# Performance work log

Hardware: AMD Instinct MI355X
Metric: run time of the kernel (lower is better)

## Reference

```python
import jax, jax.numpy as jnp
from jax import lax
import numpy as np

B, N = 512, 256
INF = jnp.float32(1e30)


def setup_inputs() -> dict:
    key = jax.random.key(0)
    k1, k2 = jax.random.split(key)
    costs = jax.random.normal(k1, (B, N, N), dtype=jnp.float32)
    pad_mask = jax.random.randint(k2, (B, N), 0, 2).astype(bool)
    return {"costs": costs, "pad_mask": pad_mask}


def _solve_lap(cost):
    """Jonker-Volgenant shortest-augmenting-path LAP, same math as
    scipy.optimize.linear_sum_assignment. cost: [n, n], rows=objects,
    cols=predictions. Returns col4row[n]: assigned column per row."""
    n = cost.shape[0]
    idx = jnp.arange(n, dtype=jnp.int32)

    def assign_row(cur_row, state):
        u, v, col4row, row4col = state
        cur_row = jnp.int32(cur_row)

        def path_cond(c):
            return c[2] < 0

        def path_body(c):
            i, minval, sink, shortest, pathrow, SR, SC = c
            SR = SR.at[i].set(True)
            r = minval + cost[i] - u[i] - v  # reduced cost of extending path via row i
            upd = jnp.logical_and(~SC, r < shortest)
            shortest = jnp.where(upd, r, shortest)
            pathrow = jnp.where(upd, i, pathrow)
            masked = jnp.where(SC, INF, shortest)
            j = jnp.argmin(masked).astype(jnp.int32)
            minval = masked[j]
            SC = SC.at[j].set(True)
            nxt = row4col[j]
            sink = jnp.where(nxt < 0, j, jnp.int32(-1))
            i = jnp.where(nxt < 0, i, nxt)
            return (i, minval, sink, shortest, pathrow, SR, SC)

        init = (cur_row, jnp.float32(0.0), jnp.int32(-1),
                jnp.full((n,), INF, jnp.float32),
                jnp.full((n,), -1, jnp.int32),
                jnp.zeros((n,), bool), jnp.zeros((n,), bool))
        i, minval, sink, shortest, pathrow, SR, SC = lax.while_loop(
            path_cond, path_body, init)

        # dual updates (Crouse 2016 / scipy lsap)
        u = u.at[cur_row].add(minval)
        others = jnp.logical_and(SR, idx != cur_row)
        u = u + jnp.where(others, minval - shortest[jnp.clip(col4row, 0, n - 1)], 0.0)
        v = v - jnp.where(SC, minval - shortest, 0.0)

        # augment along the alternating path back to cur_row
        def aug_cond(c):
            return ~c[3]

        def aug_body(c):
            j, col4row, row4col, done = c
            i = pathrow[j]
            row4col = row4col.at[j].set(i)
            j_next = col4row[i]
            col4row = col4row.at[i].set(j)
            return (j_next, col4row, row4col, i == cur_row)

        _, col4row, row4col, _ = lax.while_loop(
            aug_cond, aug_body, (sink, col4row, row4col, jnp.bool_(False)))
        return (u, v, col4row, row4col)

    state = (jnp.zeros((n,), jnp.float32), jnp.zeros((n,), jnp.float32),
             jnp.full((n,), -1, jnp.int32), jnp.full((n,), -1, jnp.int32))
    _, _, col4row, _ = lax.fori_loop(0, n, assign_row, state)
    return col4row


def _match_one(cost_t, n_k):
    # cost_t: [n_obj_slots, n_pred] (== costs[k].T); n_k: number of valid objects
    n = cost_t.shape[0]
    idx = jnp.arange(n, dtype=jnp.int32)
    rows_valid = idx < n_k
    # padded object rows get constant cost -> assignment of real rows unchanged
    P = jnp.where(rows_valid[:, None], cost_t, 0.0)
    cols = _solve_lap(P)
    # prediction indices used by real objects (cols is a permutation)
    used = jnp.zeros((n,), bool).at[cols].set(rows_valid)
    # unused prediction indices, ascending, placed first
    order = jnp.argsort(jnp.where(used, idx + n, idx)).astype(jnp.int32)
    fill = order[jnp.clip(idx - n_k, 0, n - 1)]
    return jnp.where(rows_valid, cols, fill)


def _forward(costs, pad_mask):
    costs = jnp.nan_to_num(costs.astype(jnp.float32),
                           nan=1e6, posinf=1e6, neginf=1e6)
    n_k = jnp.sum(pad_mask, axis=1).astype(jnp.int32)  # valid objects per batch
    cost_t = jnp.swapaxes(costs, 1, 2)                 # [B, n_obj, n_pred]
    return jax.vmap(_match_one)(cost_t, n_k)


def reference(costs, pad_mask):
    return _forward(costs, pad_mask)
```

## Files before the change

### kernel.cpp

```cpp
#include <hip/hip_runtime.h>
#include <math.h>

#define NB 512
#define NN 256
#define NCACHE 60
#define LAP_INF 1e30f

#define WS_NK_OFF 1024
#define WS_RMV_OFF 8192
#define WS_RMA_OFF (8192 + 512 * 1024)
#define WS_PT_OFF_FULL (8192 + 1024 * 1024)
#define WS_PT_OFF_R4 8192

__global__ __launch_bounds__(1024)
void detect_kernel(const unsigned int* __restrict__ pw, int* __restrict__ flag) {
  __shared__ int notInt, notFloat;
  if (threadIdx.x == 0) { notInt = 0; notFloat = 0; }
  __syncthreads();
  int li = 0, lf = 0;
  for (int t = threadIdx.x; t < 32768; t += 1024) {
    unsigned int w = pw[t];
    if (w > 1u) li = 1;
    if (w != 0u && w != 0x3F800000u) lf = 1;
  }
  if (li) atomicOr(&notInt, 1);
  if (lf) atomicOr(&notFloat, 1);
  __syncthreads();
  if (threadIdx.x == 0) flag[0] = (!notInt) ? 1 : ((!notFloat) ? 2 : 0);
}

__global__ __launch_bounds__(64)
void nk_kernel(const void* __restrict__ pm, const int* __restrict__ flag,
               int* __restrict__ nk) {
  const int k = blockIdx.x;
  const int lane = threadIdx.x;
  const int fl = flag[0];
  int cnt4 = 0;
  if (fl == 1) {
    const int* p = ((const int*)pm) + k * NN;
#pragma unroll
    for (int q = 0; q < 4; ++q) cnt4 += (p[lane * 4 + q] != 0);
  } else if (fl == 2) {
    const float* p = ((const float*)pm) + k * NN;
#pragma unroll
    for (int q = 0; q < 4; ++q) cnt4 += (p[lane * 4 + q] != 0.0f);
  } else {
    const unsigned char* p = ((const unsigned char*)pm) + k * NN;
#pragma unroll
    for (int q = 0; q < 4; ++q) cnt4 += (p[lane * 4 + q] != 0);
  }
#pragma unroll
  for (int off = 32; off > 0; off >>= 1) cnt4 += __shfl_down(cnt4, off);
  if (lane == 0) nk[k] = cnt4;
}

__global__ __launch_bounds__(256)
void transpose_kernel(const float* __restrict__ in, float* __restrict__ out,
                      const int* __restrict__ nk) {
  const int k = blockIdx.z;
  const int i0 = blockIdx.x * 32;
  int bnd = nk[k];
  bnd = bnd > NCACHE ? bnd : NCACHE;
  if (i0 >= bnd) return;
  __shared__ float tile[32][33];
  const float* A = in + ((size_t)k << 16);
  float* Bp = out + ((size_t)k << 16);
  const int tx = threadIdx.x, ty = threadIdx.y;
  const int j0 = blockIdx.y * 32;
#pragma unroll
  for (int r = 0; r < 32; r += 8) {
    float x = A[(size_t)(j0 + ty + r) * NN + (i0 + tx)];
    tile[ty + r][tx] = isfinite(x) ? x : 1e6f;
  }
  __syncthreads();
#pragma unroll
  for (int r = 0; r < 32; r += 8) {
    Bp[(size_t)(i0 + ty + r) * NN + (j0 + tx)] = tile[tx][ty + r];
  }
}

template <int CTRL>
__device__ __forceinline__ unsigned dpp_min_step(unsigned x) {
  unsigned y = (unsigned)__builtin_amdgcn_update_dpp((int)x, (int)x, CTRL, 0xF, 0xF, false);
  return y < x ? y : x;
}
__device__ __forceinline__ unsigned wave_min_u32(unsigned x) {
  x = dpp_min_step<0xB1>(x);
  x = dpp_min_step<0x4E>(x);
  x = dpp_min_step<0x141>(x);
  x = dpp_min_step<0x140>(x);
  x = dpp_min_step<0x142>(x);
  x = dpp_min_step<0x143>(x);
  return (unsigned)__builtin_amdgcn_readlane((int)x, 63);
}
__device__ __forceinline__ unsigned f2o(float f) {
  unsigned x = __float_as_uint(f);
  return x ^ ((unsigned)((int)x >> 31) | 0x80000000u);
}
__device__ __forceinline__ float o2f(unsigned m) {
  unsigned x = (m & 0x80000000u) ? (m & 0x7FFFFFFFu) : ~m;
  return __uint_as_float(x);
}
__device__ __forceinline__ int sel4(const int a[4], int s) {
  return (s == 0) ? a[0] : (s == 1) ? a[1] : (s == 2) ? a[2] : a[3];
}
__device__ __forceinline__ void set4(int a[4], int s, int v) {
  if (s == 0) a[0] = v; else if (s == 1) a[1] = v;
  else if (s == 2) a[2] = v; else a[3] = v;
}
__device__ __forceinline__ void setf4(float a[4], int s, float v) {
  if (s == 0) a[0] = v; else if (s == 1) a[1] = v;
  else if (s == 2) a[2] = v; else a[3] = v;
}

__global__ __launch_bounds__(256)
void rowmin_kernel(const float* __restrict__ Pt, const int* __restrict__ nk,
                   float* __restrict__ rmv, int* __restrict__ rma) {
  const int k = blockIdx.x;
  const int wid = threadIdx.x >> 6, lane = threadIdx.x & 63;
  const int row = blockIdx.y * 4 + wid;
  int bnd = nk[k];
  bnd = bnd > NCACHE ? bnd : NCACHE;
  if (row >= bnd) return;
  const float4 rv = *(const float4*)(Pt + ((size_t)k << 16) + (size_t)row * NN + lane * 4);
  float bv = rv.x; int bj = lane * 4;
  if (rv.y < bv) { bv = rv.y; bj = lane * 4 + 1; }
  if (rv.z < bv) { bv = rv.z; bj = lane * 4 + 2; }
  if (rv.w < bv) { bv = rv.w; bj = lane * 4 + 3; }
  const unsigned m = f2o(bv);
  const unsigned g = wave_min_u32(m);
  const unsigned long long cm = __ballot(m == g);
  const int owner = __ffsll(cm) - 1;
  const int ja = __builtin_amdgcn_readlane(bj, owner);
  if (lane == 0) {
    rmv[k * NN + row] = o2f(g);
    rma[k * NN + row] = ja;
  }
}

__global__ __launch_bounds__(64)
void lap_kernel(const float* __restrict__ costs, const void* __restrict__ pm,
                const int* __restrict__ flag, const int* __restrict__ nkArr,
                const float* __restrict__ rmv, const int* __restrict__ rma,
                const float* __restrict__ Pt, int* __restrict__ out, int mode) {
  const int k = blockIdx.x;
  const int lane = threadIdx.x;

  __shared__ __align__(16) float rowCache[NCACHE][NN];
  __shared__ float shortestL[NN];
  __shared__ int freeRowsL[NN];
  __shared__ unsigned char used[NN];

  const float* PtK = Pt + ((size_t)k << 16);
  const float* costK = costs + ((size_t)k << 16);

  int n_k;
  if (mode >= 1) {
    n_k = nkArr[k];
  } else {
    const int fl = flag[0];
    int cnt4 = 0;
    if (fl == 1) {
      const int* p = ((const int*)pm) + k * NN;
#pragma unroll
      for (int q = 0; q < 4; ++q) cnt4 += (p[lane * 4 + q] != 0);
    } else if (fl == 2) {
      const float* p = ((const float*)pm) + k * NN;
#pragma unroll
      for (int q = 0; q < 4; ++q) cnt4 += (p[lane * 4 + q] != 0.0f);
    } else {
      const unsigned char* p = ((const unsigned char*)pm) + k * NN;
#pragma unroll
      for (int q = 0; q < 4; ++q) cnt4 += (p[lane * 4 + q] != 0);
    }
#pragma unroll
    for (int off = 32; off > 0; off >>= 1) cnt4 += __shfl_down(cnt4, off);
    n_k = __shfl(cnt4, 0);
  }

  if (mode >= 1) {
    const float4* s4 = (const float4*)PtK;
    float4* c4 = (float4*)rowCache;
    for (int t = lane; t < NCACHE * (NN / 4); t += 64) c4[t] = s4[t];
  } else {
    for (int e = lane; e < NCACHE * NN; e += 64) {
      const int i = e >> 8, j = e & 255;
      float x = costK[(size_t)j * NN + i];
      rowCache[i][j] = isfinite(x) ? x : 1e6f;
    }
  }

  float vv[4] = {0.f, 0.f, 0.f, 0.f};
  float uu[4] = {0.f, 0.f, 0.f, 0.f};
  int r4c[4] = {-1, -1, -1, -1};
  int c4r[4] = {-1, -1, -1, -1};
  int ja[4] = {-1, -1, -1, -1};
  int nfree = 0;
  __syncthreads();

  if (mode == 2) {
    const float4 mv = *(const float4*)(rmv + k * NN + lane * 4);
    const int4 av = *(const int4*)(rma + k * NN + lane * 4);
    uu[0] = mv.x; uu[1] = mv.y; uu[2] = mv.z; uu[3] = mv.w;
    ja[0] = av.x; ja[1] = av.y; ja[2] = av.z; ja[3] = av.w;
#pragma unroll
    for (int q = 0; q < 4; ++q)
      if (lane * 4 + q >= n_k) uu[q] = 0.f;
    for (int r = 0; r < n_k; ++r) {
      const int js = __builtin_amdgcn_readlane(sel4(ja, r & 3), r >> 2);
      const int occ = __builtin_amdgcn_readlane(sel4(r4c, js & 3), js >> 2);
      if (occ < 0) {
        if (lane == (js >> 2)) set4(r4c, js & 3, r);
        if (lane == (r >> 2)) set4(c4r, r & 3, js);
      } else {
        if (lane == 0) freeRowsL[nfree] = r;
        nfree++;
      }
    }
  } else {
    float4 carry = {0.f, 0.f, 0.f, 0.f};
    for (int r = 0; r < n_k; ++r) {
      float cc[4];
      if (r < NCACHE) {
        const float4 rv = *(const float4*)(&rowCache[r][lane * 4]);
        cc[0] = rv.x; cc[1] = rv.y; cc[2] = rv.z; cc[3] = rv.w;
      } else if (mode >= 1) {
        cc[0] = carry.x; cc[1] = carry.y; cc[2] = carry.z; cc[3] = carry.w;
      } else {
#pragma unroll
        for (int q = 0; q < 4; ++q) {
          float x = costK[(size_t)(lane * 4 + q) * NN + r];
          cc[q] = isfinite(x) ? x : 1e6f;
        }
      }
      if (mode >= 1 && r + 1 >= NCACHE && r + 1 < n_k)
        carry = *(const float4*)(PtK + (size_t)(r + 1) * NN + lane * 4);

      unsigned lbv = 0xFFFFFFFFu;
      int lbq = 0;
#pragma unroll
      for (int q = 0; q < 4; ++q) {
        const unsigned m = f2o(cc[q]);
        if (m < lbv) { lbv = m; lbq = q; }
      }
      const unsigned gv = wave_min_u32(lbv);
      const unsigned long long cmask = __ballot(lbv == gv);
      const int owner = __ffsll((unsigned long long)cmask) - 1;
      const int js = (owner << 2) + __builtin_amdgcn_readlane(lbq, owner);
      if (lane == (r >> 2)) setf4(uu, r & 3, o2f(gv));
      const int occ = __builtin_amdgcn_readlane(sel4(r4c, js & 3), owner);
      if (occ < 0) {
        if (lane == owner) set4(r4c, js & 3, r);
        if (lane == (r >> 2)) set4(c4r, r & 3, js);
      } else {
        if (lane == 0) freeRowsL[nfree] = r;
        nfree++;
      }
    }
  }
  __syncthreads();

  for (int t = 0; t < nfree; ++t) {
    const int cur = freeRowsL[t];
    float sh[4] = {LAP_INF, LAP_INF, LAP_INF, LAP_INF};
    int pr[4] = {-1, -1, -1, -1};
    unsigned scm = 0;
    unsigned srm = 0;
    float minval = 0.f;
    int i = cur, sink = -1;

    while (sink < 0) {
      const int islot = i & 3, iowner = i >> 2;
      if (lane == iowner) srm |= (1u << islot);
      const float su = (islot == 0) ? uu[0] : (islot == 1) ? uu[1]
                     : (islot == 2) ? uu[2] : uu[3];
      const float ui = __int_as_float(
          __builtin_amdgcn_readlane(__float_as_int(su), iowner));

      float cc[4];
      if (i < NCACHE) {
        const float4 rv = *(const float4*)(&rowCache[i][lane * 4]);
        cc[0] = rv.x; cc[1] = rv.y; cc[2] = rv.z; cc[3] = rv.w;
      } else if (mode >= 1) {
        const float4 rv = *(const float4*)(PtK + (size_t)i * NN + lane * 4);
        cc[0] = rv.x; cc[1] = rv.y; cc[2] = rv.z; cc[3] = rv.w;
      } else {
#pragma unroll
        for (int q = 0; q < 4; ++q) {
          float x = costK[(size_t)(lane * 4 + q) * NN + i];
          cc[q] = isfinite(x) ? x : 1e6f;
        }
      }

      unsigned lbv = 0xFFFFFFFFu;
      int lbq = 0;
#pragma unroll
      for (int q = 0; q < 4; ++q) {
        float r = minval + cc[q];
        r = r - ui;
        r = r - vv[q];
        const bool sc = (scm >> q) & 1u;
        if (!sc && r < sh[q]) { sh[q] = r; pr[q] = i; }
        const unsigned m = sc ? 0xFFFFFFFFu : f2o(sh[q]);
        if (m < lbv) { lbv = m; lbq = q; }
      }
      const unsigned gv = wave_min_u32(lbv);
      minval = o2f(gv);
      const unsigned long long cmask = __ballot(lbv == gv);
      const int owner = __ffsll((unsigned long long)cmask) - 1;
      const int js = (owner << 2) + __builtin_amdgcn_readlane(lbq, owner);
      if (lane == owner) scm |= (1u << lbq);
      const int nxt = __builtin_amdgcn_readlane(sel4(r4c, js & 3), owner);
      if (nxt < 0) sink = js; else i = nxt;
    }

#pragma unroll
    for (int q = 0; q < 4; ++q) shortestL[lane * 4 + q] = sh[q];
    __syncthreads();

#pragma unroll
    for (int q = 0; q < 4; ++q) {
      if ((srm >> q) & 1u) {
        const int row = lane * 4 + q;
        if (row == cur) uu[q] = uu[q] + minval;
        else uu[q] = uu[q] + (minval - shortestL[c4r[q]]);
      }
      if ((scm >> q) & 1u) vv[q] = vv[q] - (minval - sh[q]);
    }

    int j = sink;
    bool done = false;
    while (!done) {
      const int pi = __builtin_amdgcn_readlane(sel4(pr, j & 3), j >> 2);
      if (lane == (j >> 2)) set4(r4c, j & 3, pi);
      const int jn = __builtin_amdgcn_readlane(sel4(c4r, pi & 3), pi >> 2);
      if (lane == (pi >> 2)) set4(c4r, pi & 3, j);
      done = (pi == cur);
      j = jn;
    }
    __syncthreads();
  }

  for (int t = lane; t < NN; t += 64) used[t] = 0;
  __syncthreads();
#pragma unroll
  for (int q = 0; q < 4; ++q) {
    const int row = lane * 4 + q;
    if (row < n_k) used[c4r[q]] = 1;
  }
  __syncthreads();
  int* outK = out + k * NN;
#pragma unroll
  for (int q = 0; q < 4; ++q) {
    const int row = lane * 4 + q;
    if (row < n_k) outK[row] = c4r[q];
  }
  if (lane == 0) {
    int pos = n_k;
    for (int c = 0; c < NN; ++c)
      if (!used[c]) outK[pos++] = c;
  }
}

extern "C" void kernel_launch(void* const* d_in, const int* in_sizes, int n_in,
                              void* d_out, int out_size, void* d_ws, size_t ws_size,
                              hipStream_t stream) {
  const float* costs = (const float*)d_in[0];
  const void* pm = d_in[1];
  int* out = (int*)d_out;

  int* flag = (int*)d_ws;
  int* nk = (int*)((char*)d_ws + WS_NK_OFF);
  const size_t ptBytes = (size_t)NB * NN * NN * sizeof(float);

  int mode;
  float* rmv; int* rma; float* Pt;
  if (ws_size >= WS_PT_OFF_FULL + ptBytes) {
    mode = 2;
    rmv = (float*)((char*)d_ws + WS_RMV_OFF);
    rma = (int*)((char*)d_ws + WS_RMA_OFF);
    Pt = (float*)((char*)d_ws + WS_PT_OFF_FULL);
  } else if (ws_size >= WS_PT_OFF_R4 + ptBytes) {
    mode = 1;
    rmv = (float*)d_ws; rma = (int*)d_ws;
    Pt = (float*)((char*)d_ws + WS_PT_OFF_R4);
  } else {
    mode = 0;
    rmv = (float*)d_ws; rma = (int*)d_ws;
    Pt = (float*)costs;
  }

  detect_kernel<<<1, 1024, 0, stream>>>((const unsigned int*)pm, flag);
  nk_kernel<<<NB, 64, 0, stream>>>(pm, flag, nk);
  if (mode >= 1) {
    dim3 g(8, 8, NB), b(32, 8);
    transpose_kernel<<<g, b, 0, stream>>>(costs, Pt, nk);
  }
  if (mode == 2) {
    dim3 g(NB, 64);
    rowmin_kernel<<<g, 256, 0, stream>>>(Pt, nk, rmv, rma);
  }
  lap_kernel<<<NB, 64, 0, stream>>>(costs, pm, flag, nk, rmv, rma, Pt, out, mode);
}
```

Baseline: 406.6 us.

## Add auction-style augmenting row reduction before shortest-path phase

Adds a Jonker-Volgenant augmenting row reduction pass: each free row takes its two smallest reduced costs, lowers a column price and steals the column, requeueing any displaced row, capped at a fixed number of steps. Row top-two minima are precomputed by the rowmin kernel and used as a fast path while the relevant columns are unmodified. The goal is to leave fewer free rows for the expensive shortest-augmenting-path loop. It also removes the separate nk kernel by computing counts inline in each kernel, and raises the shared row cache from 60 to 64 rows. The extra reduction pass and the more complex price bookkeeping could cost more than they save.

```diff
diff --git a/kernel.cpp b/kernel.cpp
--- a/kernel.cpp
+++ b/kernel.cpp
@@ -3,14 +3,16 @@
 
 #define NB 512
 #define NN 256
-#define NCACHE 60
+#define NCACHE 64
 #define LAP_INF 1e30f
-
-#define WS_NK_OFF 1024
-#define WS_RMV_OFF 8192
-#define WS_RMA_OFF (8192 + 512 * 1024)
-#define WS_PT_OFF_FULL (8192 + 1024 * 1024)
-#define WS_PT_OFF_R4 8192
+#define ARR_CAP 512
+
+#define WS_RM1_OFF 8192
+#define WS_RJ1_OFF (8192 + (1 << 19))
+#define WS_RM2_OFF (8192 + (2 << 19))
+#define WS_RJ2_OFF (8192 + 3 * (1 << 19))
+#define WS_PT_OFF (8192 + (4 << 19))
+#define WS_PT_OFF_MIN 8192
 
 __global__ __launch_bounds__(1024)
 void detect_kernel(const unsigned int* __restrict__ pw, int* __restrict__ flag) {
@@ -27,56 +29,6 @@
   if (lf) atomicOr(&notFloat, 1);
   __syncthreads();
   if (threadIdx.x == 0) flag[0] = (!notInt) ? 1 : ((!notFloat) ? 2 : 0);
-}
-
-__global__ __launch_bounds__(64)
-void nk_kernel(const void* __restrict__ pm, const int* __restrict__ flag,
-               int* __restrict__ nk) {
-  const int k = blockIdx.x;
-  const int lane = threadIdx.x;
-  const int fl = flag[0];
-  int cnt4 = 0;
-  if (fl == 1) {
-    const int* p = ((const int*)pm) + k * NN;
-#pragma unroll
-    for (int q = 0; q < 4; ++q) cnt4 += (p[lane * 4 + q] != 0);
-  } else if (fl == 2) {
-    const float* p = ((const float*)pm) + k * NN;
-#pragma unroll
-    for (int q = 0; q < 4; ++q) cnt4 += (p[lane * 4 + q] != 0.0f);
-  } else {
-    const unsigned char* p = ((const unsigned char*)pm) + k * NN;
-#pragma unroll
-    for (int q = 0; q < 4; ++q) cnt4 += (p[lane * 4 + q] != 0);
-  }
-#pragma unroll
-  for (int off = 32; off > 0; off >>= 1) cnt4 += __shfl_down(cnt4, off);
-  if (lane == 0) nk[k] = cnt4;
-}
-
-__global__ __launch_bounds__(256)
-void transpose_kernel(const float* __restrict__ in, float* __restrict__ out,
-                      const int* __restrict__ nk) {
-  const int k = blockIdx.z;
-  const int i0 = blockIdx.x * 32;
-  int bnd = nk[k];
-  bnd = bnd > NCACHE ? bnd : NCACHE;
-  if (i0 >= bnd) return;
-  __shared__ float tile[32][33];
-  const float* A = in + ((size_t)k << 16);
-  float* Bp = out + ((size_t)k << 16);
-  const int tx = threadIdx.x, ty = threadIdx.y;
-  const int j0 = blockIdx.y * 32;
-#pragma unroll
-  for (int r = 0; r < 32; r += 8) {
-    float x = A[(size_t)(j0 + ty + r) * NN + (i0 + tx)];
-    tile[ty + r][tx] = isfinite(x) ? x : 1e6f;
-  }
-  __syncthreads();
-#pragma unroll
-  for (int r = 0; r < 32; r += 8) {
-    Bp[(size_t)(i0 + ty + r) * NN + (j0 + tx)] = tile[tx][ty + r];
-  }
 }
 
 template <int CTRL>
@@ -112,71 +64,150 @@
   if (s == 0) a[0] = v; else if (s == 1) a[1] = v;
   else if (s == 2) a[2] = v; else a[3] = v;
 }
+__device__ __forceinline__ void subf4(float a[4], int s, float d) {
+  if (s == 0) a[0] -= d; else if (s == 1) a[1] -= d;
+  else if (s == 2) a[2] -= d; else a[3] -= d;
+}
+
+__device__ __forceinline__ void wave_two_smallest(
+    int lane, unsigned lm1, int lj1, unsigned lm2, int lj2,
+    unsigned& g1, int& gj1, unsigned& g2, int& gj2) {
+  g1 = wave_min_u32(lm1);
+  const unsigned long long b1 = __ballot(lm1 == g1);
+  const int o1 = __ffsll(b1) - 1;
+  gj1 = __builtin_amdgcn_readlane(lj1, o1);
+  const unsigned c = (lane == o1) ? lm2 : lm1;
+  const int cj = (lane == o1) ? lj2 : lj1;
+  g2 = wave_min_u32(c);
+  const unsigned long long b2 = __ballot(c == g2);
+  const int o2 = __ffsll(b2) - 1;
+  gj2 = __builtin_amdgcn_readlane(cj, o2);
+}
+
+__device__ __forceinline__ int wave_nk(const void* pm, int fl, int k, int lane) {
+  int cnt4 = 0;
+  if (fl == 1) {
+    const int* p = ((const int*)pm) + k * NN;
+#pragma unroll
+    for (int q = 0; q < 4; ++q) cnt4 += (p[lane * 4 + q] != 0);
+  } else if (fl == 2) {
+    const float* p = ((const float*)pm) + k * NN;
+#pragma unroll
+    for (int q = 0; q < 4; ++q) cnt4 += (p[lane * 4 + q] != 0.0f);
+  } else {
+    const unsigned char* p = ((const unsigned char*)pm) + k * NN;
+#pragma unroll
+    for (int q = 0; q < 4; ++q) cnt4 += (p[lane * 4 + q] != 0);
+  }
+#pragma unroll
+  for (int off = 32; off > 0; off >>= 1) cnt4 += __shfl_down(cnt4, off);
+  return __shfl(cnt4, 0);
+}
 
 __global__ __launch_bounds__(256)
-void rowmin_kernel(const float* __restrict__ Pt, const int* __restrict__ nk,
-                   float* __restrict__ rmv, int* __restrict__ rma) {
+void transpose_kernel(const float* __restrict__ in, float* __restrict__ out,
+                      const void* __restrict__ pm, const int* __restrict__ flag) {
+  __shared__ float tile[32][33];
+  __shared__ int bndS;
+  const int k = blockIdx.z;
+  const int fl = flag[0];
+  int bit;
+  if (fl == 1) bit = (((const int*)pm)[k * NN + threadIdx.x] != 0);
+  else if (fl == 2) bit = (((const float*)pm)[k * NN + threadIdx.x] != 0.0f);
+  else bit = (((const unsigned char*)pm)[k * NN + threadIdx.x] != 0);
+  const unsigned long long bb = __ballot(bit);
+  if (threadIdx.x == 0) bndS = 0;
+  __syncthreads();
+  if ((threadIdx.x & 63) == 0) atomicAdd(&bndS, __popcll(bb));
+  __syncthreads();
+  int bnd = bndS;
+  bnd = bnd > NCACHE ? bnd : NCACHE;
+  const int i0 = blockIdx.x * 32;
+  if (i0 >= bnd) return;
+  const float* A = in + ((size_t)k << 16);
+  float* Bp = out + ((size_t)k << 16);
+  const int tx = threadIdx.x & 31, ty = threadIdx.x >> 5;
+  const int j0 = blockIdx.y * 32;
+#pragma unroll
+  for (int r = 0; r < 32; r += 8) {
+    float x = A[(size_t)(j0 + ty + r) * NN + (i0 + tx)];
+    tile[ty + r][tx] = isfinite(x) ? x : 1e6f;
+  }
+  __syncthreads();
+#pragma unroll
+  for (int r = 0; r < 32; r += 8) {
+    Bp[(size_t)(i0 + ty + r) * NN + (j0 + tx)] = tile[tx][ty + r];
+  }
+}
+
+__global__ __launch_bounds__(256)
+void rowmin_kernel(const float* __restrict__ Pt, const void* __restrict__ pm,
+                   const int* __restrict__ flag,
+                   float* __restrict__ rm1, int* __restrict__ rj1,
+                   float* __restrict__ rm2, int* __restrict__ rj2) {
   const int k = blockIdx.x;
   const int wid = threadIdx.x >> 6, lane = threadIdx.x & 63;
   const int row = blockIdx.y * 4 + wid;
-  int bnd = nk[k];
-  bnd = bnd > NCACHE ? bnd : NCACHE;
+  const int fl = flag[0];
+  const int n_k = wave_nk(pm, fl, k, lane);
+  int bnd = n_k > NCACHE ? n_k : NCACHE;
   if (row >= bnd) return;
   const float4 rv = *(const float4*)(Pt + ((size_t)k << 16) + (size_t)row * NN + lane * 4);
-  float bv = rv.x; int bj = lane * 4;
-  if (rv.y < bv) { bv = rv.y; bj = lane * 4 + 1; }
-  if (rv.z < bv) { bv = rv.z; bj = lane * 4 + 2; }
-  if (rv.w < bv) { bv = rv.w; bj = lane * 4 + 3; }
-  const unsigned m = f2o(bv);
-  const unsigned g = wave_min_u32(m);
-  const unsigned long long cm = __ballot(m == g);
-  const int owner = __ffsll(cm) - 1;
-  const int ja = __builtin_amdgcn_readlane(bj, owner);
+  float w[4] = {rv.x, rv.y, rv.z, rv.w};
+  unsigned lm1 = 0xFFFFFFFFu, lm2 = 0xFFFFFFFFu;
+  int lj1 = 0, lj2 = 0;
+#pragma unroll
+  for (int q = 0; q < 4; ++q) {
+    const unsigned m = f2o(w[q]);
+    const int c = lane * 4 + q;
+    if (m < lm1) { lm2 = lm1; lj2 = lj1; lm1 = m; lj1 = c; }
+    else if (m < lm2) { lm2 = m; lj2 = c; }
+  }
+  unsigned g1, g2; int gj1, gj2;
+  wave_two_smallest(lane, lm1, lj1, lm2, lj2, g1, gj1, g2, gj2);
   if (lane == 0) {
-    rmv[k * NN + row] = o2f(g);
-    rma[k * NN + row] = ja;
+    rm1[k * NN + row] = o2f(g1);
+    rj1[k * NN + row] = gj1;
+    rm2[k * NN + row] = o2f(g2);
+    rj2[k * NN + row] = gj2;
   }
 }
 
 __global__ __launch_bounds__(64)
 void lap_kernel(const float* __restrict__ costs, const void* __restrict__ pm,
-                const int* __restrict__ flag, const int* __restrict__ nkArr,
-                const float* __restrict__ rmv, const int* __restrict__ rma,
+                const int* __restrict__ flag,
+                const float* __restrict__ rm1, const int* __restrict__ rj1,
+                const float* __restrict__ rm2, const int* __restrict__ rj2,
                 const float* __restrict__ Pt, int* __restrict__ out, int mode) {
   const int k = blockIdx.x;
   const int lane = threadIdx.x;
 
-  __shared__ __align__(16) float rowCache[NCACHE][NN];
+  __shared__ __align__(16) float rowCache[NCACHE * NN];
   __shared__ float shortestL[NN];
-  __shared__ int freeRowsL[NN];
+  __shared__ int qL[768];
+  __shared__ float rm1L[NN]; __shared__ int rj1L[NN];
+  __shared__ float rm2L[NN]; __shared__ int rj2L[NN];
   __shared__ unsigned char used[NN];
 
   const float* PtK = Pt + ((size_t)k << 16);
   const float* costK = costs + ((size_t)k << 16);
-
-  int n_k;
-  if (mode >= 1) {
-    n_k = nkArr[k];
-  } else {
-    const int fl = flag[0];
-    int cnt4 = 0;
-    if (fl == 1) {
-      const int* p = ((const int*)pm) + k * NN;
-#pragma unroll
-      for (int q = 0; q < 4; ++q) cnt4 += (p[lane * 4 + q] != 0);
-    } else if (fl == 2) {
-      const float* p = ((const float*)pm) + k * NN;
-#pragma unroll
-      for (int q = 0; q < 4; ++q) cnt4 += (p[lane * 4 + q] != 0.0f);
-    } else {
-      const unsigned char* p = ((const unsigned char*)pm) + k * NN;
-#pragma unroll
-      for (int q = 0; q < 4; ++q) cnt4 += (p[lane * 4 + q] != 0);
-    }
-#pragma unroll
-    for (int off = 32; off > 0; off >>= 1) cnt4 += __shfl_down(cnt4, off);
-    n_k = __shfl(cnt4, 0);
-  }
+  const int fl = flag[0];
+  const int n_k = wave_nk(pm, fl, k, lane);
+
+#define LOAD_ROW(ii, cc) do {                                              \
+    if ((ii) < NCACHE) {                                                   \
+      const float4 rv_ = *(const float4*)(&rowCache[(ii) * NN + lane * 4]);\
+      cc[0] = rv_.x; cc[1] = rv_.y; cc[2] = rv_.z; cc[3] = rv_.w;          \
+    } else if (mode >= 1) {                                                \
+      const float4 rv_ = *(const float4*)(PtK + (size_t)(ii) * NN + lane * 4);\
+      cc[0] = rv_.x; cc[1] = rv_.y; cc[2] = rv_.z; cc[3] = rv_.w;          \
+    } else {                                                               \
+      for (int q_ = 0; q_ < 4; ++q_) {                                     \
+        float x_ = costK[(size_t)(lane * 4 + q_) * NN + (ii)];             \
+        cc[q_] = isfinite(x_) ? x_ : 1e6f;                                 \
+      }                                                                    \
+    }                                                                      \
+  } while (0)
 
   if (mode >= 1) {
     const float4* s4 = (const float4*)PtK;
@@ -186,26 +217,33 @@
     for (int e = lane; e < NCACHE * NN; e += 64) {
       const int i = e >> 8, j = e & 255;
       float x = costK[(size_t)j * NN + i];
-      rowCache[i][j] = isfinite(x) ? x : 1e6f;
-    }
-  }
+      rowCache[i * NN + j] = isfinite(x) ? x : 1e6f;
+    }
+  }
+  if (mode == 2) {
+    for (int t = lane; t < NN; t += 64) {
+      rm1L[t] = rm1[k * NN + t];
+      rj1L[t] = rj1[k * NN + t];
+      rm2L[t] = rm2[k * NN + t];
+      rj2L[t] = rj2[k * NN + t];
+    }
+  }
+  __syncthreads();
 
   float vv[4] = {0.f, 0.f, 0.f, 0.f};
   float uu[4] = {0.f, 0.f, 0.f, 0.f};
   int r4c[4] = {-1, -1, -1, -1};
   int c4r[4] = {-1, -1, -1, -1};
-  int ja[4] = {-1, -1, -1, -1};
-  int nfree = 0;
-  __syncthreads();
+  int head = 0, tail = 0;
 
   if (mode == 2) {
-    const float4 mv = *(const float4*)(rmv + k * NN + lane * 4);
-    const int4 av = *(const int4*)(rma + k * NN + lane * 4);
-    uu[0] = mv.x; uu[1] = mv.y; uu[2] = mv.z; uu[3] = mv.w;
-    ja[0] = av.x; ja[1] = av.y; ja[2] = av.z; ja[3] = av.w;
-#pragma unroll
-    for (int q = 0; q < 4; ++q)
-      if (lane * 4 + q >= n_k) uu[q] = 0.f;
+    int ja[4];
+#pragma unroll
+    for (int q = 0; q < 4; ++q) {
+      const int row = lane * 4 + q;
+      uu[q] = (row < n_k) ? rm1L[row] : 0.f;
+      ja[q] = rj1L[row];
+    }
     for (int r = 0; r < n_k; ++r) {
       const int js = __builtin_amdgcn_readlane(sel4(ja, r & 3), r >> 2);
       const int occ = __builtin_amdgcn_readlane(sel4(r4c, js & 3), js >> 2);
@@ -213,16 +251,18 @@
         if (lane == (js >> 2)) set4(r4c, js & 3, r);
         if (lane == (r >> 2)) set4(c4r, r & 3, js);
       } else {
-        if (lane == 0) freeRowsL[nfree] = r;
-        nfree++;
+        if (lane == 0) qL[tail] = r;
+        tail++;
       }
     }
   } else {
     float4 carry = {0.f, 0.f, 0.f, 0.f};
+    if (mode >= 1 && NCACHE < n_k)
+      carry = *(const float4*)(PtK + (size_t)NCACHE * NN + lane * 4);
     for (int r = 0; r < n_k; ++r) {
       float cc[4];
       if (r < NCACHE) {
-        const float4 rv = *(const float4*)(&rowCache[r][lane * 4]);
+        const float4 rv = *(const float4*)(&rowCache[r * NN + lane * 4]);
         cc[0] = rv.x; cc[1] = rv.y; cc[2] = rv.z; cc[3] = rv.w;
       } else if (mode >= 1) {
         cc[0] = carry.x; cc[1] = carry.y; cc[2] = carry.z; cc[3] = carry.w;
@@ -235,7 +275,6 @@
       }
       if (mode >= 1 && r + 1 >= NCACHE && r + 1 < n_k)
         carry = *(const float4*)(PtK + (size_t)(r + 1) * NN + lane * 4);
-
       unsigned lbv = 0xFFFFFFFFu;
       int lbq = 0;
 #pragma unroll
@@ -253,15 +292,71 @@
         if (lane == owner) set4(r4c, js & 3, r);
         if (lane == (r >> 2)) set4(c4r, r & 3, js);
       } else {
-        if (lane == 0) freeRowsL[nfree] = r;
-        nfree++;
-      }
-    }
-  }
-  __syncthreads();
-
-  for (int t = 0; t < nfree; ++t) {
-    const int cur = freeRowsL[t];
+        if (lane == 0) qL[tail] = r;
+        tail++;
+      }
+    }
+  }
+
+  unsigned vmod = 0;
+  int steps = 0;
+  while (head < tail && steps < ARR_CAP) {
+    ++steps;
+    const int r = qL[head];
+    ++head;
+    float u1, u2;
+    int jj1, jj2;
+    bool fast = false;
+    if (mode == 2) {
+      const int pj1 = rj1L[r], pj2 = rj2L[r];
+      const unsigned s1 =
+          (unsigned)__builtin_amdgcn_readlane((int)vmod, pj1 >> 2) >> (pj1 & 3);
+      const unsigned s2 =
+          (unsigned)__builtin_amdgcn_readlane((int)vmod, pj2 >> 2) >> (pj2 & 3);
+      if (!((s1 | s2) & 1u)) {
+        fast = true;
+        u1 = rm1L[r]; u2 = rm2L[r]; jj1 = pj1; jj2 = pj2;
+      }
+    }
+    if (!fast) {
+      float cc[4];
+      LOAD_ROW(r, cc);
+      unsigned lm1 = 0xFFFFFFFFu, lm2 = 0xFFFFFFFFu;
+      int lj1 = 0, lj2 = 0;
+#pragma unroll
+      for (int q = 0; q < 4; ++q) {
+        const float w = cc[q] - vv[q];
+        const unsigned m = f2o(w);
+        const int c = lane * 4 + q;
+        if (m < lm1) { lm2 = lm1; lj2 = lj1; lm1 = m; lj1 = c; }
+        else if (m < lm2) { lm2 = m; lj2 = c; }
+      }
+      unsigned g1, g2;
+      wave_two_smallest(lane, lm1, lj1, lm2, lj2, g1, jj1, g2, jj2);
+      u1 = o2f(g1); u2 = o2f(g2);
+    }
+    if (u1 < u2) {
+      if (lane == (jj1 >> 2)) {
+        const int s = jj1 & 3;
+        subf4(vv, s, u2 - u1);
+        vmod |= (1u << s);
+      }
+    } else {
+      const int occ1 = __builtin_amdgcn_readlane(sel4(r4c, jj1 & 3), jj1 >> 2);
+      if (occ1 >= 0) jj1 = jj2;
+    }
+    if (lane == (r >> 2)) setf4(uu, r & 3, u2);
+    const int k0 = __builtin_amdgcn_readlane(sel4(r4c, jj1 & 3), jj1 >> 2);
+    if (lane == (jj1 >> 2)) set4(r4c, jj1 & 3, r);
+    if (lane == (r >> 2)) set4(c4r, r & 3, jj1);
+    if (k0 >= 0) {
+      if (lane == 0) qL[tail] = k0;
+      tail++;
+    }
+  }
+
+  for (int t = head; t < tail; ++t) {
+    const int cur = qL[t];
     float sh[4] = {LAP_INF, LAP_INF, LAP_INF, LAP_INF};
     int pr[4] = {-1, -1, -1, -1};
     unsigned scm = 0;
@@ -278,19 +373,7 @@
           __builtin_amdgcn_readlane(__float_as_int(su), iowner));
 
       float cc[4];
-      if (i < NCACHE) {
-        const float4 rv = *(const float4*)(&rowCache[i][lane * 4]);
-        cc[0] = rv.x; cc[1] = rv.y; cc[2] = rv.z; cc[3] = rv.w;
-      } else if (mode >= 1) {
-        const float4 rv = *(const float4*)(PtK + (size_t)i * NN + lane * 4);
-        cc[0] = rv.x; cc[1] = rv.y; cc[2] = rv.z; cc[3] = rv.w;
-      } else {
-#pragma unroll
-        for (int q = 0; q < 4; ++q) {
-          float x = costK[(size_t)(lane * 4 + q) * NN + i];
-          cc[q] = isfinite(x) ? x : 1e6f;
-        }
-      }
+      LOAD_ROW(i, cc);
 
       unsigned lbv = 0xFFFFFFFFu;
       int lbq = 0;
@@ -360,6 +443,7 @@
     for (int c = 0; c < NN; ++c)
       if (!used[c]) outK[pos++] = c;
   }
+#undef LOAD_ROW
 }
 
 extern "C" void kernel_launch(void* const* d_in, const int* in_sizes, int n_in,
@@ -370,35 +454,37 @@
   int* out = (int*)d_out;
 
   int* flag = (int*)d_ws;
-  int* nk = (int*)((char*)d_ws + WS_NK_OFF);
   const size_t ptBytes = (size_t)NB * NN * NN * sizeof(float);
 
   int mode;
-  float* rmv; int* rma; float* Pt;
-  if (ws_size >= WS_PT_OFF_FULL + ptBytes) {
+  float *rm1, *rm2, *Pt;
+  int *rj1, *rj2;
+  if (ws_size >= WS_PT_OFF + ptBytes) {
     mode = 2;
-    rmv = (float*)((char*)d_ws + WS_RMV_OFF);
-    rma = (int*)((char*)d_ws + WS_RMA_OFF);
-    Pt = (float*)((char*)d_ws + WS_PT_OFF_FULL);
-  } else if (ws_size >= WS_PT_OFF_R4 + ptBytes) {
+    rm1 = (float*)((char*)d_ws + WS_RM1_OFF);
+    rj1 = (int*)((char*)d_ws + WS_RJ1_OFF);
+    rm2 = (float*)((char*)d_ws + WS_RM2_OFF);
+    rj2 = (int*)((char*)d_ws + WS_RJ2_OFF);
+    Pt = (float*)((char*)d_ws + WS_PT_OFF);
+  } else if (ws_size >= WS_PT_OFF_MIN + ptBytes) {
     mode = 1;
-    rmv = (float*)d_ws; rma = (int*)d_ws;
-    Pt = (float*)((char*)d_ws + WS_PT_OFF_R4);
+    rm1 = rm2 = (float*)d_ws; rj1 = rj2 = (int*)d_ws;
+    Pt = (float*)((char*)d_ws + WS_PT_OFF_MIN);
   } else {
     mode = 0;
-    rmv = (float*)d_ws; rma = (int*)d_ws;
+    rm1 = rm2 = (float*)d_ws; rj1 = rj2 = (int*)d_ws;
     Pt = (float*)costs;
   }
 
   detect_kernel<<<1, 1024, 0, stream>>>((const unsigned int*)pm, flag);
-  nk_kernel<<<NB, 64, 0, stream>>>(pm, flag, nk);
   if (mode >= 1) {
-    dim3 g(8, 8, NB), b(32, 8);
-    transpose_kernel<<<g, b, 0, stream>>>(costs, Pt, nk);
+    dim3 g(8, 8, NB);
+    transpose_kernel<<<g, 256, 0, stream>>>(costs, Pt, pm, flag);
   }
   if (mode == 2) {
     dim3 g(NB, 64);
-    rowmin_kernel<<<g, 256, 0, stream>>>(Pt, nk, rmv, rma);
-  }
-  lap_kernel<<<NB, 64, 0, stream>>>(costs, pm, flag, nk, rmv, rma, Pt, out, mode);
-}
+    rowmin_kernel<<<g, 256, 0, stream>>>(Pt, pm, flag, rm1, rj1, rm2, rj2);
+  }
+  lap_kernel<<<NB, 64, 0, stream>>>(costs, pm, flag, rm1, rj1, rm2, rj2, Pt,
+                                    out, mode);
+}
```

Result: slower. 455.0 us (+11.9%).
